# Optimization experiments

Measured on AMD Instinct MI355X. Metric: run time of the kernel, lower is better.

Reference implementation:

```python
import jax, jax.numpy as jnp
import numpy as np

IMAGE_W = 1024
IMAGE_H = 1024
MIN_SCORE_THRESHOLD = 0.05
NMS_THRESHOLD = 0.5
MAX_DETECTION_NUM = 100


def setup_inputs() -> dict:
    key = jax.random.key(0)
    k1, k2, k3, k4 = jax.random.split(key, 4)
    B, N, C = 2, 8192, 80
    cls_heads = jax.random.uniform(k1, (B, N, C), jnp.float32)          # post-sigmoid class probs
    reg_heads = jax.random.normal(k2, (B, N, 4), jnp.float32)           # tx,ty,tw,th
    ctr = jax.random.uniform(k3, (B, N, 2), jnp.float32, 0.0, 1024.0)   # anchor centers
    wh = jax.random.uniform(k4, (B, N, 2), jnp.float32, 16.0, 256.0)    # anchor sizes
    anchors = jnp.concatenate([ctr - 0.5 * wh, ctr + 0.5 * wh], axis=-1)  # x1,y1,x2,y2
    return {"cls_heads": cls_heads, "reg_heads": reg_heads, "anchors": anchors}


def _snap_boxes(reg, anchors):
    # reg, anchors: [N, 4]
    awh = anchors[:, 2:] - anchors[:, :2]
    actr = anchors[:, :2] + 0.5 * awh
    factor = jnp.array([0.1, 0.1, 0.2, 0.2], dtype=reg.dtype)
    reg = reg * factor
    pwh = jnp.exp(reg[:, 2:]) * awh
    pctr = reg[:, :2] * awh + actr
    boxes = jnp.concatenate([pctr - 0.5 * pwh, pctr + 0.5 * pwh], axis=1)
    boxes = jax.lax.stop_gradient(boxes).astype(jnp.int32)  # torch .int() truncation
    boxes = boxes.at[:, 0].set(jnp.maximum(boxes[:, 0], 0))
    boxes = boxes.at[:, 1].set(jnp.maximum(boxes[:, 1], 0))
    boxes = boxes.at[:, 2].set(jnp.minimum(boxes[:, 2], IMAGE_W - 1))
    boxes = boxes.at[:, 3].set(jnp.minimum(boxes[:, 3], IMAGE_H - 1))
    return boxes


def _decode_one(cls_head, reg_head, anchor):
    # cls_head: [N, C], reg_head: [N, 4], anchor: [N, 4]
    scores = jnp.max(cls_head, axis=-1)
    classes = jnp.argmax(cls_head, axis=-1).astype(jnp.int32)
    boxes = _snap_boxes(reg_head, anchor)  # int32 [N,4]
    valid = scores > MIN_SCORE_THRESHOLD

    order = jnp.argsort(-scores)  # descending score order
    s = scores[order]
    c = classes[order]
    b = boxes[order]
    v = valid[order]

    bf = b.astype(jnp.float32)
    x1, y1, x2, y2 = bf[:, 0], bf[:, 1], bf[:, 2], bf[:, 3]
    area = jnp.maximum(x2 - x1, 0.0) * jnp.maximum(y2 - y1, 0.0)
    ix1 = jnp.maximum(x1[:, None], x1[None, :])
    iy1 = jnp.maximum(y1[:, None], y1[None, :])
    ix2 = jnp.minimum(x2[:, None], x2[None, :])
    iy2 = jnp.minimum(y2[:, None], y2[None, :])
    inter = jnp.maximum(ix2 - ix1, 0.0) * jnp.maximum(iy2 - iy1, 0.0)
    union = area[:, None] + area[None, :] - inter
    iou = jnp.where(union > 0.0, inter / union, 0.0)  # [N,N]

    N = s.shape[0]
    idx = jnp.arange(N)
    # class-wise suppression: box j (lower score) suppressed by kept box i if IoU>thr
    sup = (iou > NMS_THRESHOLD) & (c[:, None] == c[None, :]) & (idx[None, :] > idx[:, None])

    def body(i, keep):
        return jnp.where(keep[i], keep & ~sup[i], keep)

    keep = jax.lax.fori_loop(0, N, body, v)

    final_scores = jnp.where(keep, s, -1.0)
    top_s, top_i = jax.lax.top_k(final_scores, MAX_DETECTION_NUM)
    ok = top_s > -0.5
    out_scores = jnp.where(ok, top_s, -1.0)
    out_classes = jnp.where(ok, c[top_i], -1)
    out_boxes = jnp.where(ok[:, None], b[top_i], -1)
    return out_scores, out_classes, out_boxes


def reference(cls_heads, reg_heads, anchors):
    # cls_heads: [B,N,C], reg_heads: [B,N,4], anchors: [B,N,4]
    return jax.vmap(_decode_one)(cls_heads, reg_heads, anchors)
```

## Files before the change

kernel.cpp:

```cpp
#include <hip/hip_runtime.h>
#include <stdint.h>

#define NANCH   8192
#define NCLS    80
#define IMW     1024
#define IMH     1024
#define MAXDET  100
#define SCORE_TH 0.05f
#define TAU      0.999691f
#define CAP      512
#define KSENT    0x7FFFFFF0
#define ROWS_PB  64
#define DREPEAT  8

__device__ __forceinline__ float key_score(uint64_t key) {
    uint32_t m = (uint32_t)(key >> 32);
    uint32_t bits = (m & 0x80000000u) ? (m & 0x7FFFFFFFu) : ~m;
    return __uint_as_float(bits);
}

__global__ __launch_bounds__(256)
void decode_kernel(const float* __restrict__ cls_heads,
                   const float* __restrict__ reg_heads,
                   const float* __restrict__ anchors,
                   int* __restrict__ cnt,
                   uint64_t* __restrict__ wk,
                   uint64_t* __restrict__ wm,
                   ulonglong2* __restrict__ surv) {
    const int tid  = threadIdx.x;
    const int lane = tid & 63;
    const int part = tid & 3;
    const int b    = blockIdx.y;
    const int n    = blockIdx.x * ROWS_PB + (tid >> 2);
    const int row  = b * NANCH + n;

    for (int rep = 0; rep < DREPEAT; ++rep) {
        asm volatile("" ::: "memory");

        float best = -1e30f; int bestj = 0;
        {
            const float* rp = cls_heads + (size_t)row * NCLS;
#pragma unroll
            for (int k = 0; k < 5; ++k) {
                int j0 = part * 4 + k * 16;
                float4 v = *reinterpret_cast<const float4*>(rp + j0);
                if (v.x > best) { best = v.x; bestj = j0 + 0; }
                if (v.y > best) { best = v.y; bestj = j0 + 1; }
                if (v.z > best) { best = v.z; bestj = j0 + 2; }
                if (v.w > best) { best = v.w; bestj = j0 + 3; }
            }
        }
        uint32_t ub = __float_as_uint(best);
        uint32_t mono = (ub & 0x80000000u) ? ~ub : (ub | 0x80000000u);
        uint64_t kk = ((uint64_t)mono << 8) | (uint64_t)(255 - bestj);
        {
            uint64_t o = __shfl_xor(kk, 1); if (o > kk) kk = o;
            o = __shfl_xor(kk, 2); if (o > kk) kk = o;
        }

        bool owner = (part == 0);
        uint32_t mono32 = (uint32_t)(kk >> 8);
        int bj = 255 - (int)(kk & 0xFF);

        uint64_t key = 0, meta = 0;
        bool svv = false;
        if (owner) {
            float4 r = reinterpret_cast<const float4*>(reg_heads)[row];
            float4 a = reinterpret_cast<const float4*>(anchors)[row];

            float awx = __fsub_rn(a.z, a.x);
            float awy = __fsub_rn(a.w, a.y);
            float acx = __fadd_rn(a.x, __fmul_rn(0.5f, awx));
            float acy = __fadd_rn(a.y, __fmul_rn(0.5f, awy));
            float rx = __fmul_rn(r.x, 0.1f);
            float ry = __fmul_rn(r.y, 0.1f);
            float rw = __fmul_rn(r.z, 0.2f);
            float rh = __fmul_rn(r.w, 0.2f);
            float pwx = __fmul_rn(expf(rw), awx);
            float pwy = __fmul_rn(expf(rh), awy);
            float pcx = __fadd_rn(__fmul_rn(rx, awx), acx);
            float pcy = __fadd_rn(__fmul_rn(ry, awy), acy);

            int x1 = (int)__fsub_rn(pcx, __fmul_rn(0.5f, pwx));
            int y1 = (int)__fsub_rn(pcy, __fmul_rn(0.5f, pwy));
            int x2 = (int)__fadd_rn(pcx, __fmul_rn(0.5f, pwx));
            int y2 = (int)__fadd_rn(pcy, __fmul_rn(0.5f, pwy));
            x1 = max(x1, 0);
            y1 = max(y1, 0);
            x2 = min(x2, IMW - 1);
            y2 = min(y2, IMH - 1);

            key = ((uint64_t)mono32 << 32)
                | ((uint64_t)((~(uint32_t)n) & 0xFFFFu) << 16)
                | (uint64_t)(uint32_t)bj;
            meta = (uint64_t)(uint16_t)x1
                 | ((uint64_t)(uint16_t)y1 << 16)
                 | ((uint64_t)(uint16_t)x2 << 32)
                 | ((uint64_t)(uint16_t)y2 << 48);

            wk[row] = key;
            wm[row] = meta;

            uint32_t mono_tau = __float_as_uint(TAU) | 0x80000000u;
            svv = (mono32 > mono_tau);
        }

        if (rep == DREPEAT - 1) {
            uint64_t mask = __ballot(svv);
            int rank = __popcll(mask & ((1ULL << lane) - 1ULL));
            int base = 0;
            if (lane == 0 && mask) base = atomicAdd(cnt + b, __popcll(mask));
            base = __shfl(base, 0);
            if (svv) {
                int p = base + rank;
                if (p < CAP) surv[(size_t)b * CAP + p] = make_ulonglong2(key, meta);
            }
        }
    }
}

struct Kept {
    float x1[2], y1[2], x2[2], y2[2], ar[2];
    int   cl[2];
};

__device__ __forceinline__ void nms_try_keep(uint64_t key, uint64_t meta, float s,
                                             int lane, int& nk, Kept& K,
                                             float* __restrict__ out, int b) {
    int cls = (int)(key & 0xFFFFu);
    float cx1 = (float)(short)(meta & 0xFFFFu);
    float cy1 = (float)(short)((meta >> 16) & 0xFFFFu);
    float cx2 = (float)(short)((meta >> 32) & 0xFFFFu);
    float cy2 = (float)(short)((meta >> 48) & 0xFFFFu);
    float ca = fmaxf(cx2 - cx1, 0.f) * fmaxf(cy2 - cy1, 0.f);

    bool supp = false;
#pragma unroll
    for (int r = 0; r < 2; ++r) {
        int slot = lane + 64 * r;
        if (slot < nk && K.cl[r] == cls) {
            float ix1 = fmaxf(K.x1[r], cx1), iy1 = fmaxf(K.y1[r], cy1);
            float ix2 = fminf(K.x2[r], cx2), iy2 = fminf(K.y2[r], cy2);
            float inter = fmaxf(ix2 - ix1, 0.f) * fmaxf(iy2 - iy1, 0.f);
            if (3.f * inter > K.ar[r] + ca) supp = true;
        }
    }
    if (__ballot(supp) != 0ULL) return;

    int rr = nk >> 6, l = nk & 63;
    if (lane == l) {
        if (rr == 0) { K.x1[0]=cx1; K.y1[0]=cy1; K.x2[0]=cx2; K.y2[0]=cy2; K.ar[0]=ca; K.cl[0]=cls; }
        else         { K.x1[1]=cx1; K.y1[1]=cy1; K.x2[1]=cx2; K.y2[1]=cy2; K.ar[1]=ca; K.cl[1]=cls; }
    }
    if (lane == 0) {
        out[b * MAXDET + nk] = s;
        out[2 * MAXDET + b * MAXDET + nk] = (float)cls;
        float* ob = out + 4 * MAXDET + (size_t)(b * MAXDET + nk) * 4;
        ob[0] = cx1; ob[1] = cy1; ob[2] = cx2; ob[3] = cy2;
    }
    ++nk;
}

__global__ __launch_bounds__(256)
void sort_nms_kernel(const int* __restrict__ cnt,
                     const uint64_t* __restrict__ wk,
                     const uint64_t* __restrict__ wm,
                     const ulonglong2* __restrict__ surv,
                     float* __restrict__ out) {
    __shared__ __align__(16) ulonglong2 sv_[CAP];
    __shared__ __align__(16) ulonglong2 sq[CAP];
    __shared__ __align__(16) uint64_t skey[CAP + 16];
    __shared__ float4 kept_box[128];
    __shared__ float  kept_area[128];
    __shared__ int    kept_cls[128];
    __shared__ uint64_t smask[4];
    __shared__ uint64_t sby[4 * 64];
    __shared__ int snk, sdone, sneedfb;
    __shared__ uint64_t fbmap[NANCH / 64];

    const int b = blockIdx.x;
    const int tid = threadIdx.x;
    const int lane = tid & 63;
    const int w = tid >> 6;

    ulonglong2 v0 = surv[(size_t)b * CAP + tid];
    ulonglong2 v1 = surv[(size_t)b * CAP + 256 + tid];
    int c = cnt[b];

    bool overflow = (c > CAP) || (c < 0);
    if (overflow) c = 0;
    const int cpad   = (c + 63) & ~63;
    const int cpad16 = (c + 15) & ~15;

    sv_[tid]       = v0;  skey[tid]       = (tid < c)       ? v0.x : 0ULL;
    sv_[256 + tid] = v1;  skey[256 + tid] = (256 + tid < c) ? v1.x : 0ULL;
    if (tid < 128) kept_cls[tid] = KSENT;
    if (tid == 0) { snk = 0; sdone = 0; sneedfb = overflow ? 1 : 0; }
    __syncthreads();

    for (int i = tid; i < c; i += 256) {
        uint64_t ky = skey[i];
        int r = 0;
        for (int j0 = 0; j0 < cpad16; j0 += 16) {
            int acc = 0;
#pragma unroll
            for (int u = 0; u < 8; ++u) {
                ulonglong2 pr = *reinterpret_cast<const ulonglong2*>(&skey[j0 + 2 * u]);
                acc += (int)(pr.x > ky) + (int)(pr.y > ky);
            }
            r += acc;
        }
        sq[r] = sv_[i];
    }
    for (int i = c + tid; i < cpad; i += 256) sq[i] = make_ulonglong2(0ULL, 0ULL);

    for (int p0 = 0; p0 < cpad; p0 += 64) {
        __syncthreads();
        if (sdone) break;
        const int nk = snk;

        ulonglong2 kv = sq[p0 + lane];
        uint64_t key = kv.x, meta = kv.y;
        float s = key_score(key);
        bool sval = (s > SCORE_TH);
        int cls_c = sval ? (int)(key & 0xFFFFu) : -1;
        float cx1 = (float)(short)(meta & 0xFFFFu);
        float cy1 = (float)(short)((meta >> 16) & 0xFFFFu);
        float cx2 = (float)(short)((meta >> 32) & 0xFFFFu);
        float cy2 = (float)(short)((meta >> 48) & 0xFFFFu);
        float ca = fmaxf(cx2 - cx1, 0.f) * fmaxf(cy2 - cy1, 0.f);

        bool supk = false;
        int kp = (((nk + 3) >> 2) + 7) & ~7;
        for (int k0 = 0; k0 < kp; k0 += 8) {
#pragma unroll
            for (int u = 0; u < 8; ++u) {
                int j = w + 4 * (k0 + u);
                float4 kb = kept_box[j];
                float ka = kept_area[j];
                int kc = kept_cls[j];
                float ix1 = fmaxf(kb.x, cx1), iy1 = fmaxf(kb.y, cy1);
                float ix2 = fminf(kb.z, cx2), iy2 = fminf(kb.w, cy2);
                float inter = fmaxf(ix2 - ix1, 0.f) * fmaxf(iy2 - iy1, 0.f);
                supk |= (kc == cls_c) & (3.f * inter > ka + ca);
            }
        }

        uint64_t sbyw = 0;
#pragma unroll
        for (int u = 0; u < 16; ++u) {
            int t = (w << 4) + u;
            ulonglong2 tv = sq[p0 + t];
            uint64_t tkey = tv.x, tmeta = tv.y;
            float ts = key_score(tkey);
            int tcls = (int)(tkey & 0xFFFFu);
            float tx1 = (float)(short)(tmeta & 0xFFFFu);
            float ty1 = (float)(short)((tmeta >> 16) & 0xFFFFu);
            float tx2 = (float)(short)((tmeta >> 32) & 0xFFFFu);
            float ty2 = (float)(short)((tmeta >> 48) & 0xFFFFu);
            float ta = fmaxf(tx2 - tx1, 0.f) * fmaxf(ty2 - ty1, 0.f);
            float ix1 = fmaxf(tx1, cx1), iy1 = fmaxf(ty1, cy1);
            float ix2 = fminf(tx2, cx2), iy2 = fminf(ty2, cy2);
            float inter = fmaxf(ix2 - ix1, 0.f) * fmaxf(iy2 - iy1, 0.f);
            bool sup = (t < lane) && (ts > SCORE_TH) && (tcls == cls_c)
                       && (3.f * inter > ta + ca);
            sbyw |= ((uint64_t)sup) << t;
        }

        uint64_t mk = __ballot(supk);
        if (lane == 0) smask[w] = mk;
        sby[(w << 6) + lane] = sbyw;
        __syncthreads();

        if (w == 0) {
            uint64_t supkAll = smask[0] | smask[1] | smask[2] | smask[3];
            uint64_t supBy = sby[lane] | sby[64 + lane] | sby[128 + lane] | sby[192 + lane];
            bool alive0 = sval && !((supkAll >> lane) & 1ULL);

            uint64_t aliveCand = __ballot(alive0);
            uint64_t aliveMask;
            if (__ballot(supBy != 0ULL) == 0ULL) {
                aliveMask = aliveCand;
            } else {
                uint64_t killed = 0;
                for (int t = 0; t < 64; ++t) {
                    uint64_t kill_t = __ballot((supBy >> t) & 1ULL);
                    bool talive = ((aliveCand >> t) & 1ULL) && !((killed >> t) & 1ULL);
                    if (talive) killed |= kill_t;
                }
                aliveMask = aliveCand & ~killed;
            }

            int myrank = __popcll(aliveMask & ((1ULL << lane) - 1ULL));
            bool keepme = ((aliveMask >> lane) & 1ULL) && (nk + myrank < MAXDET);
            if (keepme) {
                int slot = nk + myrank;
                kept_box[slot]  = make_float4(cx1, cy1, cx2, cy2);
                kept_area[slot] = ca;
                kept_cls[slot]  = cls_c;
                out[b * MAXDET + slot] = s;
                out[2 * MAXDET + b * MAXDET + slot] = (float)cls_c;
                float* ob = out + 4 * MAXDET + (size_t)(b * MAXDET + slot) * 4;
                ob[0] = cx1; ob[1] = cy1; ob[2] = cx2; ob[3] = cy2;
            }
            int navail = __popcll(aliveMask);
            int room = MAXDET - nk;
            int nk2 = nk + ((navail < room) ? navail : room);
            uint64_t invalid = __ballot(!sval);
            if (lane == 0) {
                snk = nk2;
                if (nk2 >= MAXDET) sdone = 1;
                else if (invalid) { sneedfb = 1; sdone = 1; }
            }
        }
    }
    __syncthreads();

    int nk = snk;
    bool need_fb = sneedfb || (!sdone && nk < MAXDET);

    if (tid >= 64) return;

    if (need_fb) {
        const uint64_t* wkb = wk + (size_t)b * NANCH;
        const uint64_t* wmb = wm + (size_t)b * NANCH;
        for (int i = lane; i < NANCH / 64; i += 64) fbmap[i] = 0ULL;
        __builtin_amdgcn_wave_barrier();

        nk = 0;
        Kept K;
        K.cl[0] = K.cl[1] = -1;
        K.x1[0]=K.y1[0]=K.x2[0]=K.y2[0]=K.ar[0]=0.f;
        K.x1[1]=K.y1[1]=K.x2[1]=K.y2[1]=K.ar[1]=0.f;

        for (int iter = 0; iter < NANCH; ++iter) {
            uint64_t mybest = 0; int myq = -1;
            for (int q = lane; q < NANCH; q += 64) {
                bool cons = (fbmap[q >> 6] >> (q & 63)) & 1ULL;
                uint64_t kk2 = wkb[q];
                if (!cons && kk2 > mybest) { mybest = kk2; myq = q; }
            }
            uint64_t best2 = mybest;
#pragma unroll
            for (int j = 32; j; j >>= 1) {
                uint64_t o = __shfl_xor(best2, j);
                if (o > best2) best2 = o;
            }
            if (best2 == 0ULL) break;
            float s = key_score(best2);
            if (!(s > SCORE_TH)) break;
            uint64_t msk = __ballot(mybest == best2);
            int wl = __ffsll((unsigned long long)msk) - 1;
            int q = __shfl(myq, wl);
            if (lane == wl) fbmap[q >> 6] |= (1ULL << (q & 63));
            uint64_t cm = wmb[q];
            nms_try_keep(best2, cm, s, lane, nk, K, out, b);
            if (nk == MAXDET) break;
            __builtin_amdgcn_wave_barrier();
        }
    }

    for (int t = nk + lane; t < MAXDET; t += 64) {
        out[b * MAXDET + t] = -1.f;
        out[2 * MAXDET + b * MAXDET + t] = -1.f;
        float* ob = out + 4 * MAXDET + (size_t)(b * MAXDET + t) * 4;
        ob[0] = -1.f; ob[1] = -1.f; ob[2] = -1.f; ob[3] = -1.f;
    }
}

extern "C" void kernel_launch(void* const* d_in, const int* in_sizes, int n_in,
                              void* d_out, int out_size, void* d_ws, size_t ws_size,
                              hipStream_t stream) {
    (void)in_sizes; (void)n_in; (void)out_size; (void)ws_size;
    const float* cls_heads = (const float*)d_in[0];
    const float* reg_heads = (const float*)d_in[1];
    const float* anchors   = (const float*)d_in[2];
    float* out = (float*)d_out;

    char* w = (char*)d_ws;
    int*        cnt  = (int*)w;
    uint64_t*   wk   = (uint64_t*)(w + 1024);
    uint64_t*   wm   = (uint64_t*)(w + 1024 + 131072);
    ulonglong2* surv = (ulonglong2*)(w + 1024 + 262144);

    hipMemsetAsync(cnt, 0, 2 * sizeof(int), stream);
    decode_kernel<<<dim3(NANCH / ROWS_PB, 2), 256, 0, stream>>>(cls_heads, reg_heads, anchors,
                                                                cnt, wk, wm, surv);
    sort_nms_kernel<<<dim3(2), 256, 0, stream>>>(cnt, wk, wm, surv, out);
}
```

Baseline: 28.13 us.

## Drop repeated decode, decode boxes only for survivors, defer full decode to fallback

The decode kernel no longer runs its body eight times. It now does the box regression and the global reads of reg/anchors only for anchors whose top score passes the survivor threshold. The full per-anchor key/meta arrays are no longer written on every run; they are rebuilt inside the sort/NMS kernel only when the fallback path is needed. The rank-sort loop also computes two keys per thread in one pass over shared memory, and the staging copy in shared memory is removed. The cost is that the rare fallback path becomes slower, since two blocks must redo the 8192-anchor decode serially.

```diff
diff --git a/kernel.cpp b/kernel.cpp
--- a/kernel.cpp
+++ b/kernel.cpp
@@ -11,12 +11,45 @@
 #define CAP      512
 #define KSENT    0x7FFFFFF0
 #define ROWS_PB  64
-#define DREPEAT  8
 
 __device__ __forceinline__ float key_score(uint64_t key) {
     uint32_t m = (uint32_t)(key >> 32);
     uint32_t bits = (m & 0x80000000u) ? (m & 0x7FFFFFFFu) : ~m;
     return __uint_as_float(bits);
+}
+
+__device__ __forceinline__ void decode_one(const float4 r, const float4 a,
+                                           uint32_t mono32, int bj, int n,
+                                           uint64_t& key, uint64_t& meta) {
+    float awx = __fsub_rn(a.z, a.x);
+    float awy = __fsub_rn(a.w, a.y);
+    float acx = __fadd_rn(a.x, __fmul_rn(0.5f, awx));
+    float acy = __fadd_rn(a.y, __fmul_rn(0.5f, awy));
+    float rx = __fmul_rn(r.x, 0.1f);
+    float ry = __fmul_rn(r.y, 0.1f);
+    float rw = __fmul_rn(r.z, 0.2f);
+    float rh = __fmul_rn(r.w, 0.2f);
+    float pwx = __fmul_rn(expf(rw), awx);
+    float pwy = __fmul_rn(expf(rh), awy);
+    float pcx = __fadd_rn(__fmul_rn(rx, awx), acx);
+    float pcy = __fadd_rn(__fmul_rn(ry, awy), acy);
+
+    int x1 = (int)__fsub_rn(pcx, __fmul_rn(0.5f, pwx));
+    int y1 = (int)__fsub_rn(pcy, __fmul_rn(0.5f, pwy));
+    int x2 = (int)__fadd_rn(pcx, __fmul_rn(0.5f, pwx));
+    int y2 = (int)__fadd_rn(pcy, __fmul_rn(0.5f, pwy));
+    x1 = max(x1, 0);
+    y1 = max(y1, 0);
+    x2 = min(x2, IMW - 1);
+    y2 = min(y2, IMH - 1);
+
+    key = ((uint64_t)mono32 << 32)
+        | ((uint64_t)((~(uint32_t)n) & 0xFFFFu) << 16)
+        | (uint64_t)(uint32_t)bj;
+    meta = (uint64_t)(uint16_t)x1
+         | ((uint64_t)(uint16_t)y1 << 16)
+         | ((uint64_t)(uint16_t)x2 << 32)
+         | ((uint64_t)(uint16_t)y2 << 48);
 }
 
 __global__ __launch_bounds__(256)
@@ -24,8 +57,6 @@
                    const float* __restrict__ reg_heads,
                    const float* __restrict__ anchors,
                    int* __restrict__ cnt,
-                   uint64_t* __restrict__ wk,
-                   uint64_t* __restrict__ wm,
                    ulonglong2* __restrict__ surv) {
     const int tid  = threadIdx.x;
     const int lane = tid & 63;
@@ -34,88 +65,49 @@
     const int n    = blockIdx.x * ROWS_PB + (tid >> 2);
     const int row  = b * NANCH + n;
 
-    for (int rep = 0; rep < DREPEAT; ++rep) {
-        asm volatile("" ::: "memory");
-
-        float best = -1e30f; int bestj = 0;
-        {
-            const float* rp = cls_heads + (size_t)row * NCLS;
-#pragma unroll
-            for (int k = 0; k < 5; ++k) {
-                int j0 = part * 4 + k * 16;
-                float4 v = *reinterpret_cast<const float4*>(rp + j0);
-                if (v.x > best) { best = v.x; bestj = j0 + 0; }
-                if (v.y > best) { best = v.y; bestj = j0 + 1; }
-                if (v.z > best) { best = v.z; bestj = j0 + 2; }
-                if (v.w > best) { best = v.w; bestj = j0 + 3; }
-            }
-        }
-        uint32_t ub = __float_as_uint(best);
-        uint32_t mono = (ub & 0x80000000u) ? ~ub : (ub | 0x80000000u);
-        uint64_t kk = ((uint64_t)mono << 8) | (uint64_t)(255 - bestj);
-        {
-            uint64_t o = __shfl_xor(kk, 1); if (o > kk) kk = o;
-            o = __shfl_xor(kk, 2); if (o > kk) kk = o;
-        }
-
-        bool owner = (part == 0);
+    float best = -1e30f; int bestj = 0;
+    {
+        const float* rp = cls_heads + (size_t)row * NCLS;
+#pragma unroll
+        for (int k = 0; k < 5; ++k) {
+            int j0 = part * 4 + k * 16;
+            float4 v = *reinterpret_cast<const float4*>(rp + j0);
+            if (v.x > best) { best = v.x; bestj = j0 + 0; }
+            if (v.y > best) { best = v.y; bestj = j0 + 1; }
+            if (v.z > best) { best = v.z; bestj = j0 + 2; }
+            if (v.w > best) { best = v.w; bestj = j0 + 3; }
+        }
+    }
+    uint32_t ub = __float_as_uint(best);
+    uint32_t mono = (ub & 0x80000000u) ? ~ub : (ub | 0x80000000u);
+    uint64_t kk = ((uint64_t)mono << 8) | (uint64_t)(255 - bestj);
+    {
+        uint64_t o = __shfl_xor(kk, 1); if (o > kk) kk = o;
+        o = __shfl_xor(kk, 2); if (o > kk) kk = o;
+    }
+
+    uint64_t key = 0, meta = 0;
+    bool svv = false;
+    if (part == 0) {
         uint32_t mono32 = (uint32_t)(kk >> 8);
-        int bj = 255 - (int)(kk & 0xFF);
-
-        uint64_t key = 0, meta = 0;
-        bool svv = false;
-        if (owner) {
+        uint32_t mono_tau = __float_as_uint(TAU) | 0x80000000u;
+        if (mono32 > mono_tau) {
+            int bj = 255 - (int)(kk & 0xFF);
             float4 r = reinterpret_cast<const float4*>(reg_heads)[row];
             float4 a = reinterpret_cast<const float4*>(anchors)[row];
-
-            float awx = __fsub_rn(a.z, a.x);
-            float awy = __fsub_rn(a.w, a.y);
-            float acx = __fadd_rn(a.x, __fmul_rn(0.5f, awx));
-            float acy = __fadd_rn(a.y, __fmul_rn(0.5f, awy));
-            float rx = __fmul_rn(r.x, 0.1f);
-            float ry = __fmul_rn(r.y, 0.1f);
-            float rw = __fmul_rn(r.z, 0.2f);
-            float rh = __fmul_rn(r.w, 0.2f);
-            float pwx = __fmul_rn(expf(rw), awx);
-            float pwy = __fmul_rn(expf(rh), awy);
-            float pcx = __fadd_rn(__fmul_rn(rx, awx), acx);
-            float pcy = __fadd_rn(__fmul_rn(ry, awy), acy);
-
-            int x1 = (int)__fsub_rn(pcx, __fmul_rn(0.5f, pwx));
-            int y1 = (int)__fsub_rn(pcy, __fmul_rn(0.5f, pwy));
-            int x2 = (int)__fadd_rn(pcx, __fmul_rn(0.5f, pwx));
-            int y2 = (int)__fadd_rn(pcy, __fmul_rn(0.5f, pwy));
-            x1 = max(x1, 0);
-            y1 = max(y1, 0);
-            x2 = min(x2, IMW - 1);
-            y2 = min(y2, IMH - 1);
-
-            key = ((uint64_t)mono32 << 32)
-                | ((uint64_t)((~(uint32_t)n) & 0xFFFFu) << 16)
-                | (uint64_t)(uint32_t)bj;
-            meta = (uint64_t)(uint16_t)x1
-                 | ((uint64_t)(uint16_t)y1 << 16)
-                 | ((uint64_t)(uint16_t)x2 << 32)
-                 | ((uint64_t)(uint16_t)y2 << 48);
-
-            wk[row] = key;
-            wm[row] = meta;
-
-            uint32_t mono_tau = __float_as_uint(TAU) | 0x80000000u;
-            svv = (mono32 > mono_tau);
-        }
-
-        if (rep == DREPEAT - 1) {
-            uint64_t mask = __ballot(svv);
-            int rank = __popcll(mask & ((1ULL << lane) - 1ULL));
-            int base = 0;
-            if (lane == 0 && mask) base = atomicAdd(cnt + b, __popcll(mask));
-            base = __shfl(base, 0);
-            if (svv) {
-                int p = base + rank;
-                if (p < CAP) surv[(size_t)b * CAP + p] = make_ulonglong2(key, meta);
-            }
-        }
+            decode_one(r, a, mono32, bj, n, key, meta);
+            svv = true;
+        }
+    }
+
+    uint64_t mask = __ballot(svv);
+    int rank = __popcll(mask & ((1ULL << lane) - 1ULL));
+    int base = 0;
+    if (lane == 0 && mask) base = atomicAdd(cnt + b, __popcll(mask));
+    base = __shfl(base, 0);
+    if (svv) {
+        int p = base + rank;
+        if (p < CAP) surv[(size_t)b * CAP + p] = make_ulonglong2(key, meta);
     }
 }
 
@@ -163,11 +155,13 @@
 
 __global__ __launch_bounds__(256)
 void sort_nms_kernel(const int* __restrict__ cnt,
-                     const uint64_t* __restrict__ wk,
-                     const uint64_t* __restrict__ wm,
+                     const float* __restrict__ cls_heads,
+                     const float* __restrict__ reg_heads,
+                     const float* __restrict__ anchors,
+                     uint64_t* __restrict__ wk,
+                     uint64_t* __restrict__ wm,
                      const ulonglong2* __restrict__ surv,
                      float* __restrict__ out) {
-    __shared__ __align__(16) ulonglong2 sv_[CAP];
     __shared__ __align__(16) ulonglong2 sq[CAP];
     __shared__ __align__(16) uint64_t skey[CAP + 16];
     __shared__ float4 kept_box[128];
@@ -192,25 +186,28 @@
     const int cpad   = (c + 63) & ~63;
     const int cpad16 = (c + 15) & ~15;
 
-    sv_[tid]       = v0;  skey[tid]       = (tid < c)       ? v0.x : 0ULL;
-    sv_[256 + tid] = v1;  skey[256 + tid] = (256 + tid < c) ? v1.x : 0ULL;
+    skey[tid]       = (tid < c)       ? v0.x : 0ULL;
+    skey[256 + tid] = (256 + tid < c) ? v1.x : 0ULL;
     if (tid < 128) kept_cls[tid] = KSENT;
     if (tid == 0) { snk = 0; sdone = 0; sneedfb = overflow ? 1 : 0; }
     __syncthreads();
 
-    for (int i = tid; i < c; i += 256) {
-        uint64_t ky = skey[i];
-        int r = 0;
-        for (int j0 = 0; j0 < cpad16; j0 += 16) {
-            int acc = 0;
-#pragma unroll
-            for (int u = 0; u < 8; ++u) {
-                ulonglong2 pr = *reinterpret_cast<const ulonglong2*>(&skey[j0 + 2 * u]);
-                acc += (int)(pr.x > ky) + (int)(pr.y > ky);
-            }
-            r += acc;
-        }
-        sq[r] = sv_[i];
+    {
+        bool h0 = tid < c, h1 = 256 + tid < c;
+        if (h0 | h1) {
+            uint64_t k0 = v0.x, k1 = v1.x;
+            int r0 = 0, r1 = 0;
+            for (int j0 = 0; j0 < cpad16; j0 += 16) {
+#pragma unroll
+                for (int u = 0; u < 8; ++u) {
+                    ulonglong2 pr = *reinterpret_cast<const ulonglong2*>(&skey[j0 + 2 * u]);
+                    r0 += (int)(pr.x > k0) + (int)(pr.y > k0);
+                    r1 += (int)(pr.x > k1) + (int)(pr.y > k1);
+                }
+            }
+            if (h0) sq[r0] = v0;
+            if (h1) sq[r1] = v1;
+        }
     }
     for (int i = c + tid; i < cpad; i += 256) sq[i] = make_ulonglong2(0ULL, 0ULL);
 
@@ -319,6 +316,29 @@
     int nk = snk;
     bool need_fb = sneedfb || (!sdone && nk < MAXDET);
 
+    if (need_fb) {
+        uint64_t* wkb = wk + (size_t)b * NANCH;
+        uint64_t* wmb = wm + (size_t)b * NANCH;
+        for (int n2 = tid; n2 < NANCH; n2 += 256) {
+            int row2 = b * NANCH + n2;
+            const float* rp = cls_heads + (size_t)row2 * NCLS;
+            float best = -1e30f; int bj = 0;
+            for (int j = 0; j < NCLS; ++j) {
+                float v = rp[j];
+                if (v > best) { best = v; bj = j; }
+            }
+            uint32_t ub = __float_as_uint(best);
+            uint32_t mono32 = (ub & 0x80000000u) ? ~ub : (ub | 0x80000000u);
+            float4 r = reinterpret_cast<const float4*>(reg_heads)[row2];
+            float4 a = reinterpret_cast<const float4*>(anchors)[row2];
+            uint64_t key2, meta2;
+            decode_one(r, a, mono32, bj, n2, key2, meta2);
+            wkb[n2] = key2;
+            wmb[n2] = meta2;
+        }
+        __syncthreads();
+    }
+
     if (tid >= 64) return;
 
     if (need_fb) {
@@ -385,6 +405,7 @@
 
     hipMemsetAsync(cnt, 0, 2 * sizeof(int), stream);
     decode_kernel<<<dim3(NANCH / ROWS_PB, 2), 256, 0, stream>>>(cls_heads, reg_heads, anchors,
-                                                                cnt, wk, wm, surv);
-    sort_nms_kernel<<<dim3(2), 256, 0, stream>>>(cnt, wk, wm, surv, out);
-}
+                                                                cnt, surv);
+    sort_nms_kernel<<<dim3(2), 256, 0, stream>>>(cnt, cls_heads, reg_heads, anchors,
+                                                 wk, wm, surv, out);
+}
```

Measured after the change: 25.34 us. 1.11x faster.
